# Kernel optimization log

Hardware: AMD Instinct MI355X
Metric: run time of the kernel (lower is better)

## Reference

```python
import jax, jax.numpy as jnp
import numpy as np

B, T, C, H = 2, 2048, 1024, 16
HD = C // H          # head dim = 64
HD2 = HD // 2        # rotary half = 32


def setup_inputs() -> dict:
    key = jax.random.key(0)
    k0, k1, k2 = jax.random.split(key, 3)
    x = jax.random.normal(k0, (B, T, C), jnp.float32)
    Wqkv = jax.random.normal(k1, (C, 3 * C), jnp.float32) * (1.0 / np.sqrt(C))
    bqkv = jnp.zeros((3 * C,), jnp.float32)
    Wproj = jax.random.normal(k2, (C, C), jnp.float32) * (1.0 / np.sqrt(C))
    bproj = jnp.zeros((C,), jnp.float32)
    # standard rotary frequencies: theta_i = 10000^{-2i/hd}
    inv_freq = 1.0 / (10000.0 ** (jnp.arange(0, HD, 2, dtype=jnp.float32) / HD))
    angles = jnp.arange(T, dtype=jnp.float32)[:, None] * inv_freq[None, :]  # (T, HD2)
    return {
        "x": x,
        "freqs_cos": jnp.cos(angles),
        "freqs_sin": jnp.sin(angles),
        "Wqkv": Wqkv,
        "bqkv": bqkv,
        "Wproj": Wproj,
        "bproj": bproj,
    }


def _rope(u, cos, sin):
    # u: (B, T, H, HD); half-split pairing: (u[i], u[i + HD/2]) form a complex pair
    u1, u2 = u[..., :HD2], u[..., HD2:]
    c = cos[None, :, None, :]  # (1, T, 1, HD2)
    s = sin[None, :, None, :]
    return jnp.concatenate([u1 * c - u2 * s, u1 * s + u2 * c], axis=-1)


def reference(x, freqs_cos, freqs_sin, Wqkv, bqkv, Wproj, bproj):
    Bc, Tc, Cc = x.shape
    qkv = x @ Wqkv + bqkv                      # (B, T, 3C)
    q, k, v = jnp.split(qkv, 3, axis=-1)
    q = q.reshape(Bc, Tc, H, HD)
    k = k.reshape(Bc, Tc, H, HD)
    v = v.reshape(Bc, Tc, H, HD)
    q = _rope(q, freqs_cos, freqs_sin)
    k = _rope(k, freqs_cos, freqs_sin)
    scale = 1.0 / np.sqrt(HD)
    scores = jnp.einsum("bthd,bshd->bhts", q, k) * scale  # (B, H, T, T)
    causal = jnp.tril(jnp.ones((Tc, Tc), dtype=bool))
    scores = jnp.where(causal[None, None], scores, jnp.finfo(scores.dtype).min)
    p = jax.nn.softmax(scores, axis=-1)
    y = jnp.einsum("bhts,bshd->bthd", p, v).reshape(Bc, Tc, Cc)
    return y @ Wproj + bproj
```

## Files before the change

kernel.cpp:

```cpp
#include <hip/hip_runtime.h>
#include <hip/hip_bf16.h>
#include <cstdint>
#include <cmath>

typedef __bf16 bf16_t;
typedef __attribute__((ext_vector_type(8))) __bf16 bf16x8;
typedef __attribute__((ext_vector_type(4))) float f32x4;

#define LOG2E 1.4426950408889634f

constexpr int B_ = 2, T_ = 2048, C_ = 1024, H_ = 16, HD_ = 64, HD2_ = 32;
constexpr int M_ = B_ * T_;

static __device__ __forceinline__ f32x4 mfma16(bf16x8 a, bf16x8 b, f32x4 c) {
    return __builtin_amdgcn_mfma_f32_16x16x32_bf16(a, b, c, 0, 0, 0);
}

#define GLL(gp, lp)                                                          \
    __builtin_amdgcn_global_load_lds(                                        \
        (const __attribute__((address_space(1))) void*)(gp),                 \
        (__attribute__((address_space(3))) void*)(lp), 16, 0, 0)

__global__ void cast_f32_to_bf16(const float* __restrict__ in, bf16_t* __restrict__ out, int n4) {
    int i = blockIdx.x * blockDim.x + threadIdx.x;
    if (i < n4) {
        float4 v = ((const float4*)in)[i];
        bf16_t o[4] = {(bf16_t)v.x, (bf16_t)v.y, (bf16_t)v.z, (bf16_t)v.w};
        *(uint64_t*)(out + (size_t)i * 4) = *(uint64_t*)o;
    }
}

__global__ void transpose_cast(const float* __restrict__ W, bf16_t* __restrict__ WT, int K, int N) {
    __shared__ float tile[32][33];
    int nb = blockIdx.x * 32, kb = blockIdx.y * 32;
    for (int i = threadIdx.y; i < 32; i += 8)
        tile[i][threadIdx.x] = W[(size_t)(kb + i) * N + nb + threadIdx.x];
    __syncthreads();
    for (int i = threadIdx.y; i < 32; i += 8)
        WT[(size_t)(nb + i) * K + kb + threadIdx.x] = (bf16_t)tile[threadIdx.x][i];
}

template <int MODE>
__global__ __launch_bounds__(256, 2) void gemm128(
    const bf16_t* __restrict__ A, const bf16_t* __restrict__ BT, const float* __restrict__ bias,
    int N, int K,
    bf16_t* __restrict__ Qb, bf16_t* __restrict__ Kb, bf16_t* __restrict__ VTb,
    const float* __restrict__ cosT, const float* __restrict__ sinT, float* __restrict__ out) {
    __shared__ alignas(16) bf16_t As[128 * 32];
    __shared__ alignas(16) bf16_t Bs[128 * 32];
    const int tid = threadIdx.x;
    const int w = tid >> 6, lane = tid & 63;
    const int quad = lane >> 4, r = lane & 15;
    const int wm = (w >> 1) * 64, wn = (w & 1) * 64;
    const int mb = blockIdx.y * 128, nb = blockIdx.x * 128;
    const int row_st = tid >> 2, seg = tid & 3;

    f32x4 acc[4][4] = {};

    const bf16_t* gA0 = A + (size_t)(mb + row_st) * K + seg * 8;
    const bf16_t* gA1 = A + (size_t)(mb + row_st + 64) * K + seg * 8;
    const bf16_t* gB0 = BT + (size_t)(nb + row_st) * K + seg * 8;
    const bf16_t* gB1 = BT + (size_t)(nb + row_st + 64) * K + seg * 8;

    for (int k0 = 0; k0 < K; k0 += 32) {
        __syncthreads();
        GLL(gA0 + k0, As + tid * 8);
        GLL(gA1 + k0, As + 2048 + tid * 8);
        GLL(gB0 + k0, Bs + tid * 8);
        GLL(gB1 + k0, Bs + 2048 + tid * 8);
        __syncthreads();
        bf16x8 af[4], bfr[4];
#pragma unroll
        for (int i = 0; i < 4; i++) af[i] = *(const bf16x8*)(As + (wm + i * 16 + r) * 32 + quad * 8);
#pragma unroll
        for (int j = 0; j < 4; j++) bfr[j] = *(const bf16x8*)(Bs + (wn + j * 16 + r) * 32 + quad * 8);
#pragma unroll
        for (int i = 0; i < 4; i++)
#pragma unroll
            for (int j = 0; j < 4; j++) acc[i][j] = mfma16(af[i], bfr[j], acc[i][j]);
    }

    if (MODE == 0) {
        const int col_base = nb + wn;
        const int region = col_base >> 10;
        const int h = (col_base & 1023) >> 6;
        const float qscale = 0.125f * LOG2E;
        if (region < 2) {
#pragma unroll
            for (int i = 0; i < 4; i++) {
#pragma unroll
                for (int g = 0; g < 4; g++) {
                    int m = mb + wm + i * 16 + quad * 4 + g;
                    int b = m >> 11, t = m & (T_ - 1);
                    bf16_t* dst = (region == 0 ? Qb : Kb) + ((size_t)((b * H_ + h) * T_ + t)) * 64;
                    int tw = t & 7;
#pragma unroll
                    for (int j = 0; j < 2; j++) {
                        int d = j * 16 + r;
                        float u1 = acc[i][j][g] + bias[col_base + d];
                        float u2 = acc[i][j + 2][g] + bias[col_base + d + 32];
                        float c = cosT[t * HD2_ + d], s = sinT[t * HD2_ + d];
                        float o1 = u1 * c - u2 * s;
                        float o2 = u1 * s + u2 * c;
                        if (region == 0) {
                            dst[d] = (bf16_t)(o1 * qscale);
                            dst[d + 32] = (bf16_t)(o2 * qscale);
                        } else {
                            dst[((((d >> 3) ^ tw)) << 3) | (d & 7)] = (bf16_t)o1;
                            dst[(((((d + 32) >> 3) ^ tw)) << 3) | (d & 7)] = (bf16_t)o2;
                        }
                    }
                }
            }
        } else {
#pragma unroll
            for (int i = 0; i < 4; i++) {
                int m0 = mb + wm + i * 16 + quad * 4;
                int b = m0 >> 11, t0 = m0 & (T_ - 1);
                bf16_t* base = VTb + (size_t)(b * H_ + h) * 64 * T_;
#pragma unroll
                for (int j = 0; j < 4; j++) {
                    int d = j * 16 + r;
                    float bb = bias[col_base + d];
                    bf16_t pk[4];
#pragma unroll
                    for (int g = 0; g < 4; g++) pk[g] = (bf16_t)(acc[i][j][g] + bb);
                    int c = (((t0 >> 3) & 7) ^ (d & 7));
                    int tsw = (t0 & ~63) | (c << 3) | (t0 & 7);
                    *(uint64_t*)(base + (size_t)d * T_ + tsw) = *(uint64_t*)pk;
                }
            }
        }
    } else {
#pragma unroll
        for (int i = 0; i < 4; i++)
#pragma unroll
            for (int g = 0; g < 4; g++) {
                int m = mb + wm + i * 16 + quad * 4 + g;
#pragma unroll
                for (int j = 0; j < 4; j++) {
                    int col = nb + wn + j * 16 + r;
                    out[(size_t)m * N + col] = acc[i][j][g] + bias[col];
                }
            }
    }
}

__global__ __launch_bounds__(256, 2) void attn64(
    const bf16_t* __restrict__ Qb, const bf16_t* __restrict__ Kb,
    const bf16_t* __restrict__ VTb, bf16_t* __restrict__ att) {
    __shared__ alignas(16) bf16_t Ks[2][64 * 64];
    __shared__ alignas(16) bf16_t Vs[2][64 * 64];
    __shared__ alignas(16) bf16_t Ps[4][1024];
    const int tid = threadIdx.x;
    const int w = tid >> 6, lane = tid & 63;
    const int quad = lane >> 4, r = lane & 15;
    const int pt = blockIdx.x;
    const int bh = blockIdx.y;
    const size_t kbase = (size_t)bh * T_ * 64;
    const size_t vbase = (size_t)bh * 64 * T_;
    bf16_t* Pw = &Ps[w][0];
    const int srow = tid >> 3, schunk = tid & 7;
    const int koff0 = ((quad ^ (r & 7)) * 8);
    const int koff1 = (((quad + 4) ^ (r & 7)) * 8);

    for (int half = 0; half < 2; half++) {
        const int qt = half ? (31 - pt) : pt;
        const int q0 = qt * 64;
        const int qrow = q0 + w * 16 + r;
        bf16x8 qf0 = *(const bf16x8*)(Qb + kbase + (size_t)qrow * 64 + quad * 8);
        bf16x8 qf1 = *(const bf16x8*)(Qb + kbase + (size_t)qrow * 64 + 32 + quad * 8);
        f32x4 oacc[4] = {};
        float mstate = -INFINITY, lstate = 0.f;
        const int n = qt + 1;

        __syncthreads();
        {
            const bf16_t* kg = Kb + kbase + (size_t)srow * 64 + schunk * 8;
            GLL(kg, &Ks[0][0] + tid * 8);
            GLL(kg + 32 * 64, &Ks[0][0] + 2048 + tid * 8);
            const bf16_t* vg = VTb + vbase + (size_t)srow * T_ + schunk * 8;
            GLL(vg, &Vs[0][0] + tid * 8);
            GLL(vg + (size_t)32 * T_, &Vs[0][0] + 2048 + tid * 8);
        }
        for (int jt = 0; jt < n; jt++) {
            const int cur = jt & 1;
            const int j0 = jt * 64;
            __syncthreads();
            if (jt + 1 < n) {
                const int j0n = j0 + 64;
                const bf16_t* kg = Kb + kbase + (size_t)(j0n + srow) * 64 + schunk * 8;
                GLL(kg, &Ks[cur ^ 1][0] + tid * 8);
                GLL(kg + 32 * 64, &Ks[cur ^ 1][0] + 2048 + tid * 8);
                const bf16_t* vg = VTb + vbase + (size_t)srow * T_ + j0n + schunk * 8;
                GLL(vg, &Vs[cur ^ 1][0] + tid * 8);
                GLL(vg + (size_t)32 * T_, &Vs[cur ^ 1][0] + 2048 + tid * 8);
            }
            f32x4 s[4];
#pragma unroll
            for (int m0 = 0; m0 < 4; m0++) {
                const bf16_t* kp = &Ks[cur][(m0 * 16 + r) * 64];
                bf16x8 kf0 = *(const bf16x8*)(kp + koff0);
                bf16x8 kf1 = *(const bf16x8*)(kp + koff1);
                f32x4 z = {0.f, 0.f, 0.f, 0.f};
                z = mfma16(kf0, qf0, z);
                z = mfma16(kf1, qf1, z);
                s[m0] = z;
            }
            if (jt == qt) {
#pragma unroll
                for (int m0 = 0; m0 < 4; m0++) {
                    int kvb = j0 + m0 * 16 + quad * 4;
#pragma unroll
                    for (int g = 0; g < 4; g++)
                        if (kvb + g > qrow) s[m0][g] = -INFINITY;
                }
            }
            float vm = -INFINITY;
#pragma unroll
            for (int m0 = 0; m0 < 4; m0++)
#pragma unroll
                for (int g = 0; g < 4; g++) vm = fmaxf(vm, s[m0][g]);
            vm = fmaxf(vm, __shfl_xor(vm, 16));
            vm = fmaxf(vm, __shfl_xor(vm, 32));
            float mnew = fmaxf(mstate, vm);
            float alpha = __builtin_amdgcn_exp2f(mstate - mnew);
            float rs = 0.f;
#pragma unroll
            for (int m0 = 0; m0 < 4; m0++)
#pragma unroll
                for (int g = 0; g < 4; g++) {
                    float p = __builtin_amdgcn_exp2f(s[m0][g] - mnew);
                    s[m0][g] = p;
                    rs += p;
                }
            rs += __shfl_xor(rs, 16);
            rs += __shfl_xor(rs, 32);
            lstate = lstate * alpha + rs;
            mstate = mnew;
#pragma unroll
            for (int d0 = 0; d0 < 4; d0++)
#pragma unroll
                for (int g = 0; g < 4; g++) oacc[d0][g] *= alpha;
#pragma unroll
            for (int m0 = 0; m0 < 4; m0++) {
                bf16_t hq[4];
#pragma unroll
                for (int g = 0; g < 4; g++) hq[g] = (bf16_t)s[m0][g];
                int elem = (m0 >> 1) * 512 + (((m0 & 1) * 2 + (quad >> 1)) * 16 + r) * 8 + (quad & 1) * 4;
                *(uint64_t*)(Pw + elem) = *(uint64_t*)hq;
            }
            __builtin_amdgcn_wave_barrier();
            bf16x8 pf0 = *(const bf16x8*)(Pw + lane * 8);
            bf16x8 pf1 = *(const bf16x8*)(Pw + 512 + lane * 8);
#pragma unroll
            for (int d0 = 0; d0 < 4; d0++) {
                const bf16_t* vp = &Vs[cur][(d0 * 16 + r) * 64];
                bf16x8 vf0 = *(const bf16x8*)(vp + koff0);
                bf16x8 vf1 = *(const bf16x8*)(vp + koff1);
                oacc[d0] = mfma16(vf0, pf0, oacc[d0]);
                oacc[d0] = mfma16(vf1, pf1, oacc[d0]);
            }
            __builtin_amdgcn_wave_barrier();
        }
        int b = bh >> 4, h = bh & 15;
        float inv = 1.f / lstate;
        bf16_t* dst = att + ((size_t)(b * T_ + qrow)) * 1024 + h * 64;
#pragma unroll
        for (int d0 = 0; d0 < 4; d0++) {
            bf16_t hh[4];
#pragma unroll
            for (int g = 0; g < 4; g++) hh[g] = (bf16_t)(oacc[d0][g] * inv);
            *(uint64_t*)(dst + d0 * 16 + quad * 4) = *(uint64_t*)hh;
        }
    }
}

extern "C" void kernel_launch(void* const* d_in, const int* in_sizes, int n_in,
                              void* d_out, int out_size, void* d_ws, size_t ws_size,
                              hipStream_t stream) {
    const float* x = (const float*)d_in[0];
    const float* fcos = (const float*)d_in[1];
    const float* fsin = (const float*)d_in[2];
    const float* Wqkv = (const float*)d_in[3];
    const float* bqkv = (const float*)d_in[4];
    const float* Wproj = (const float*)d_in[5];
    const float* bproj = (const float*)d_in[6];
    float* out = (float*)d_out;

    uint8_t* p = (uint8_t*)d_ws;
    size_t need = 0;
    auto take = [&](size_t bytes) {
        void* q = p;
        size_t pad = (bytes + 255) & ~(size_t)255;
        p += pad;
        need += pad;
        return q;
    };
    bf16_t* xb = (bf16_t*)take((size_t)M_ * C_ * 2);
    bf16_t* wqkvT = (bf16_t*)take((size_t)3 * C_ * C_ * 2);
    bf16_t* wprojT = (bf16_t*)take((size_t)C_ * C_ * 2);
    bf16_t* Qb = (bf16_t*)take((size_t)B_ * H_ * T_ * 64 * 2);
    bf16_t* Kb = (bf16_t*)take((size_t)B_ * H_ * T_ * 64 * 2);
    bf16_t* VTb = (bf16_t*)take((size_t)B_ * H_ * 64 * T_ * 2);
    bf16_t* attb = (bf16_t*)take((size_t)M_ * C_ * 2);
    if (ws_size < need) return;

    cast_f32_to_bf16<<<(M_ * C_ / 4 + 255) / 256, 256, 0, stream>>>(x, xb, M_ * C_ / 4);
    transpose_cast<<<dim3(3 * C_ / 32, C_ / 32), dim3(32, 8), 0, stream>>>(Wqkv, wqkvT, C_, 3 * C_);
    transpose_cast<<<dim3(C_ / 32, C_ / 32), dim3(32, 8), 0, stream>>>(Wproj, wprojT, C_, C_);

    gemm128<0><<<dim3(3 * C_ / 128, M_ / 128), 256, 0, stream>>>(
        xb, wqkvT, bqkv, 3 * C_, C_, Qb, Kb, VTb, fcos, fsin, nullptr);

    attn64<<<dim3(16, B_ * H_), 256, 0, stream>>>(Qb, Kb, VTb, attb);

    gemm128<1><<<dim3(C_ / 128, M_ / 128), 256, 0, stream>>>(
        attb, wprojT, bproj, C_, C_, nullptr, nullptr, nullptr, nullptr, nullptr, out);
}
```

Before: 204.7 us.

## Process paired query tiles together in attention and merge prep kernels

The attention kernel now handles its two causal-balanced query tiles (pt and 31-pt) in one shared pass over K/V tiles. Each staged K/V tile is reused for both query tiles, so the shorter tile's K/V loads and barriers are no longer repeated. The grid is flattened and remapped so that the heads sharing an XCD index are grouped, which is meant to improve L2 locality. The three preprocessing kernels (x cast and two weight transposes) are merged into one launch. In exchange, each thread holds more live registers for two sets of accumulators, and the P scratch buffer in LDS doubles.

```diff
diff --git a/kernel.cpp b/kernel.cpp
--- a/kernel.cpp
+++ b/kernel.cpp
@@ -21,23 +21,36 @@
         (const __attribute__((address_space(1))) void*)(gp),                 \
         (__attribute__((address_space(3))) void*)(lp), 16, 0, 0)
 
-__global__ void cast_f32_to_bf16(const float* __restrict__ in, bf16_t* __restrict__ out, int n4) {
-    int i = blockIdx.x * blockDim.x + threadIdx.x;
-    if (i < n4) {
-        float4 v = ((const float4*)in)[i];
+__global__ void prep(const float* __restrict__ x, bf16_t* __restrict__ xb,
+                     const float* __restrict__ Wqkv, bf16_t* __restrict__ wqkvT,
+                     const float* __restrict__ Wproj, bf16_t* __restrict__ wprojT) {
+    __shared__ float tile[32][33];
+    const int bid = blockIdx.x, tid = threadIdx.x;
+    if (bid < 4096) {
+        int i = bid * 256 + tid;
+        float4 v = ((const float4*)x)[i];
         bf16_t o[4] = {(bf16_t)v.x, (bf16_t)v.y, (bf16_t)v.z, (bf16_t)v.w};
-        *(uint64_t*)(out + (size_t)i * 4) = *(uint64_t*)o;
-    }
-}
-
-__global__ void transpose_cast(const float* __restrict__ W, bf16_t* __restrict__ WT, int K, int N) {
-    __shared__ float tile[32][33];
-    int nb = blockIdx.x * 32, kb = blockIdx.y * 32;
-    for (int i = threadIdx.y; i < 32; i += 8)
-        tile[i][threadIdx.x] = W[(size_t)(kb + i) * N + nb + threadIdx.x];
+        *(uint64_t*)(xb + (size_t)i * 4) = *(uint64_t*)o;
+        return;
+    }
+    const float* W;
+    bf16_t* WT;
+    int K, N, nb, kb;
+    if (bid < 4096 + 3072) {
+        int t = bid - 4096;
+        W = Wqkv; WT = wqkvT; K = C_; N = 3 * C_;
+        nb = (t % 96) * 32; kb = (t / 96) * 32;
+    } else {
+        int t = bid - 7168;
+        W = Wproj; WT = wprojT; K = C_; N = C_;
+        nb = (t & 31) * 32; kb = (t >> 5) * 32;
+    }
+    int tx = tid & 31, ty = tid >> 5;
+    for (int i = ty; i < 32; i += 8)
+        tile[i][tx] = W[(size_t)(kb + i) * N + nb + tx];
     __syncthreads();
-    for (int i = threadIdx.y; i < 32; i += 8)
-        WT[(size_t)(nb + i) * K + kb + threadIdx.x] = (bf16_t)tile[threadIdx.x][i];
+    for (int i = ty; i < 32; i += 8)
+        WT[(size_t)(nb + i) * K + kb + tx] = (bf16_t)tile[tx][i];
 }
 
 template <int MODE>
@@ -151,126 +164,186 @@
     const bf16_t* __restrict__ VTb, bf16_t* __restrict__ att) {
     __shared__ alignas(16) bf16_t Ks[2][64 * 64];
     __shared__ alignas(16) bf16_t Vs[2][64 * 64];
-    __shared__ alignas(16) bf16_t Ps[4][1024];
+    __shared__ alignas(16) bf16_t Ps[4][2048];
     const int tid = threadIdx.x;
     const int w = tid >> 6, lane = tid & 63;
     const int quad = lane >> 4, r = lane & 15;
-    const int pt = blockIdx.x;
-    const int bh = blockIdx.y;
+    const int idx = blockIdx.x;
+    const int xcd = idx & 7, jj = idx >> 3;
+    const int bh = (jj >> 4) * 8 + xcd;
+    const int pt = jj & 15;
+    const int qtA = pt, qtB = 31 - pt;
     const size_t kbase = (size_t)bh * T_ * 64;
     const size_t vbase = (size_t)bh * 64 * T_;
-    bf16_t* Pw = &Ps[w][0];
+    bf16_t* PwB = &Ps[w][0];
+    bf16_t* PwA = &Ps[w][1024];
     const int srow = tid >> 3, schunk = tid & 7;
     const int koff0 = ((quad ^ (r & 7)) * 8);
     const int koff1 = (((quad + 4) ^ (r & 7)) * 8);
 
-    for (int half = 0; half < 2; half++) {
-        const int qt = half ? (31 - pt) : pt;
-        const int q0 = qt * 64;
-        const int qrow = q0 + w * 16 + r;
-        bf16x8 qf0 = *(const bf16x8*)(Qb + kbase + (size_t)qrow * 64 + quad * 8);
-        bf16x8 qf1 = *(const bf16x8*)(Qb + kbase + (size_t)qrow * 64 + 32 + quad * 8);
-        f32x4 oacc[4] = {};
-        float mstate = -INFINITY, lstate = 0.f;
-        const int n = qt + 1;
-
+    const int qrowA = qtA * 64 + w * 16 + r;
+    const int qrowB = qtB * 64 + w * 16 + r;
+    bf16x8 qfA0 = *(const bf16x8*)(Qb + kbase + (size_t)qrowA * 64 + quad * 8);
+    bf16x8 qfA1 = *(const bf16x8*)(Qb + kbase + (size_t)qrowA * 64 + 32 + quad * 8);
+    bf16x8 qfB0 = *(const bf16x8*)(Qb + kbase + (size_t)qrowB * 64 + quad * 8);
+    bf16x8 qfB1 = *(const bf16x8*)(Qb + kbase + (size_t)qrowB * 64 + 32 + quad * 8);
+
+    f32x4 oaccA[4] = {}, oaccB[4] = {};
+    float mA = -INFINITY, lA = 0.f, mB = -INFINITY, lB = 0.f;
+
+    auto stageKV = [&](int jt, int buf) {
+        const bf16_t* kg = Kb + kbase + (size_t)(jt * 64 + srow) * 64 + schunk * 8;
+        GLL(kg, &Ks[buf][0] + tid * 8);
+        GLL(kg + 32 * 64, &Ks[buf][0] + 2048 + tid * 8);
+        const bf16_t* vg = VTb + vbase + (size_t)srow * T_ + jt * 64 + schunk * 8;
+        GLL(vg, &Vs[buf][0] + tid * 8);
+        GLL(vg + (size_t)32 * T_, &Vs[buf][0] + 2048 + tid * 8);
+    };
+    auto softmax = [&](f32x4* s, float& m, float& l, f32x4* oacc) {
+        float vm = -INFINITY;
+#pragma unroll
+        for (int m0 = 0; m0 < 4; m0++)
+#pragma unroll
+            for (int g = 0; g < 4; g++) vm = fmaxf(vm, s[m0][g]);
+        vm = fmaxf(vm, __shfl_xor(vm, 16));
+        vm = fmaxf(vm, __shfl_xor(vm, 32));
+        float mnew = fmaxf(m, vm);
+        float alpha = __builtin_amdgcn_exp2f(m - mnew);
+        float rs = 0.f;
+#pragma unroll
+        for (int m0 = 0; m0 < 4; m0++)
+#pragma unroll
+            for (int g = 0; g < 4; g++) {
+                float pp = __builtin_amdgcn_exp2f(s[m0][g] - mnew);
+                s[m0][g] = pp;
+                rs += pp;
+            }
+        rs += __shfl_xor(rs, 16);
+        rs += __shfl_xor(rs, 32);
+        l = l * alpha + rs;
+        m = mnew;
+#pragma unroll
+        for (int d0 = 0; d0 < 4; d0++)
+#pragma unroll
+            for (int g = 0; g < 4; g++) oacc[d0][g] *= alpha;
+    };
+    auto packP = [&](f32x4* s, bf16_t* Pw) {
+#pragma unroll
+        for (int m0 = 0; m0 < 4; m0++) {
+            bf16_t hq[4];
+#pragma unroll
+            for (int g = 0; g < 4; g++) hq[g] = (bf16_t)s[m0][g];
+            int elem = (m0 >> 1) * 512 + (((m0 & 1) * 2 + (quad >> 1)) * 16 + r) * 8 + (quad & 1) * 4;
+            *(uint64_t*)(Pw + elem) = *(uint64_t*)hq;
+        }
+    };
+
+    stageKV(0, 0);
+    for (int jt = 0; jt <= qtB; jt++) {
+        const int cur = jt & 1;
+        const int j0 = jt * 64;
         __syncthreads();
-        {
-            const bf16_t* kg = Kb + kbase + (size_t)srow * 64 + schunk * 8;
-            GLL(kg, &Ks[0][0] + tid * 8);
-            GLL(kg + 32 * 64, &Ks[0][0] + 2048 + tid * 8);
-            const bf16_t* vg = VTb + vbase + (size_t)srow * T_ + schunk * 8;
-            GLL(vg, &Vs[0][0] + tid * 8);
-            GLL(vg + (size_t)32 * T_, &Vs[0][0] + 2048 + tid * 8);
-        }
-        for (int jt = 0; jt < n; jt++) {
-            const int cur = jt & 1;
-            const int j0 = jt * 64;
-            __syncthreads();
-            if (jt + 1 < n) {
-                const int j0n = j0 + 64;
-                const bf16_t* kg = Kb + kbase + (size_t)(j0n + srow) * 64 + schunk * 8;
-                GLL(kg, &Ks[cur ^ 1][0] + tid * 8);
-                GLL(kg + 32 * 64, &Ks[cur ^ 1][0] + 2048 + tid * 8);
-                const bf16_t* vg = VTb + vbase + (size_t)srow * T_ + j0n + schunk * 8;
-                GLL(vg, &Vs[cur ^ 1][0] + tid * 8);
-                GLL(vg + (size_t)32 * T_, &Vs[cur ^ 1][0] + 2048 + tid * 8);
-            }
-            f32x4 s[4];
+        if (jt < qtB) stageKV(jt + 1, cur ^ 1);
+        const bool doA = (jt <= qtA);
+
+        f32x4 sA[4], sB[4];
+        if (doA) {
 #pragma unroll
             for (int m0 = 0; m0 < 4; m0++) {
                 const bf16_t* kp = &Ks[cur][(m0 * 16 + r) * 64];
                 bf16x8 kf0 = *(const bf16x8*)(kp + koff0);
                 bf16x8 kf1 = *(const bf16x8*)(kp + koff1);
-                f32x4 z = {0.f, 0.f, 0.f, 0.f};
-                z = mfma16(kf0, qf0, z);
-                z = mfma16(kf1, qf1, z);
-                s[m0] = z;
-            }
-            if (jt == qt) {
-#pragma unroll
-                for (int m0 = 0; m0 < 4; m0++) {
-                    int kvb = j0 + m0 * 16 + quad * 4;
-#pragma unroll
-                    for (int g = 0; g < 4; g++)
-                        if (kvb + g > qrow) s[m0][g] = -INFINITY;
-                }
-            }
-            float vm = -INFINITY;
-#pragma unroll
-            for (int m0 = 0; m0 < 4; m0++)
-#pragma unroll
-                for (int g = 0; g < 4; g++) vm = fmaxf(vm, s[m0][g]);
-            vm = fmaxf(vm, __shfl_xor(vm, 16));
-            vm = fmaxf(vm, __shfl_xor(vm, 32));
-            float mnew = fmaxf(mstate, vm);
-            float alpha = __builtin_amdgcn_exp2f(mstate - mnew);
-            float rs = 0.f;
-#pragma unroll
-            for (int m0 = 0; m0 < 4; m0++)
-#pragma unroll
-                for (int g = 0; g < 4; g++) {
-                    float p = __builtin_amdgcn_exp2f(s[m0][g] - mnew);
-                    s[m0][g] = p;
-                    rs += p;
-                }
-            rs += __shfl_xor(rs, 16);
-            rs += __shfl_xor(rs, 32);
-            lstate = lstate * alpha + rs;
-            mstate = mnew;
-#pragma unroll
-            for (int d0 = 0; d0 < 4; d0++)
-#pragma unroll
-                for (int g = 0; g < 4; g++) oacc[d0][g] *= alpha;
+                f32x4 zB = {0.f, 0.f, 0.f, 0.f};
+                zB = mfma16(kf0, qfB0, zB);
+                zB = mfma16(kf1, qfB1, zB);
+                sB[m0] = zB;
+                f32x4 zA = {0.f, 0.f, 0.f, 0.f};
+                zA = mfma16(kf0, qfA0, zA);
+                zA = mfma16(kf1, qfA1, zA);
+                sA[m0] = zA;
+            }
+        } else {
 #pragma unroll
             for (int m0 = 0; m0 < 4; m0++) {
-                bf16_t hq[4];
-#pragma unroll
-                for (int g = 0; g < 4; g++) hq[g] = (bf16_t)s[m0][g];
-                int elem = (m0 >> 1) * 512 + (((m0 & 1) * 2 + (quad >> 1)) * 16 + r) * 8 + (quad & 1) * 4;
-                *(uint64_t*)(Pw + elem) = *(uint64_t*)hq;
-            }
-            __builtin_amdgcn_wave_barrier();
-            bf16x8 pf0 = *(const bf16x8*)(Pw + lane * 8);
-            bf16x8 pf1 = *(const bf16x8*)(Pw + 512 + lane * 8);
+                const bf16_t* kp = &Ks[cur][(m0 * 16 + r) * 64];
+                bf16x8 kf0 = *(const bf16x8*)(kp + koff0);
+                bf16x8 kf1 = *(const bf16x8*)(kp + koff1);
+                f32x4 zB = {0.f, 0.f, 0.f, 0.f};
+                zB = mfma16(kf0, qfB0, zB);
+                zB = mfma16(kf1, qfB1, zB);
+                sB[m0] = zB;
+            }
+        }
+        if (jt == qtB) {
+#pragma unroll
+            for (int m0 = 0; m0 < 4; m0++) {
+                int kvb = j0 + m0 * 16 + quad * 4;
+#pragma unroll
+                for (int g = 0; g < 4; g++)
+                    if (kvb + g > qrowB) sB[m0][g] = -INFINITY;
+            }
+        }
+        if (jt == qtA) {
+#pragma unroll
+            for (int m0 = 0; m0 < 4; m0++) {
+                int kvb = j0 + m0 * 16 + quad * 4;
+#pragma unroll
+                for (int g = 0; g < 4; g++)
+                    if (kvb + g > qrowA) sA[m0][g] = -INFINITY;
+            }
+        }
+        softmax(sB, mB, lB, oaccB);
+        if (doA) softmax(sA, mA, lA, oaccA);
+        packP(sB, PwB);
+        if (doA) packP(sA, PwA);
+        __builtin_amdgcn_wave_barrier();
+        bf16x8 pfB0 = *(const bf16x8*)(PwB + lane * 8);
+        bf16x8 pfB1 = *(const bf16x8*)(PwB + 512 + lane * 8);
+        if (doA) {
+            bf16x8 pfA0 = *(const bf16x8*)(PwA + lane * 8);
+            bf16x8 pfA1 = *(const bf16x8*)(PwA + 512 + lane * 8);
 #pragma unroll
             for (int d0 = 0; d0 < 4; d0++) {
                 const bf16_t* vp = &Vs[cur][(d0 * 16 + r) * 64];
                 bf16x8 vf0 = *(const bf16x8*)(vp + koff0);
                 bf16x8 vf1 = *(const bf16x8*)(vp + koff1);
-                oacc[d0] = mfma16(vf0, pf0, oacc[d0]);
-                oacc[d0] = mfma16(vf1, pf1, oacc[d0]);
-            }
-            __builtin_amdgcn_wave_barrier();
-        }
-        int b = bh >> 4, h = bh & 15;
-        float inv = 1.f / lstate;
-        bf16_t* dst = att + ((size_t)(b * T_ + qrow)) * 1024 + h * 64;
+                oaccB[d0] = mfma16(vf0, pfB0, oaccB[d0]);
+                oaccB[d0] = mfma16(vf1, pfB1, oaccB[d0]);
+                oaccA[d0] = mfma16(vf0, pfA0, oaccA[d0]);
+                oaccA[d0] = mfma16(vf1, pfA1, oaccA[d0]);
+            }
+        } else {
+#pragma unroll
+            for (int d0 = 0; d0 < 4; d0++) {
+                const bf16_t* vp = &Vs[cur][(d0 * 16 + r) * 64];
+                bf16x8 vf0 = *(const bf16x8*)(vp + koff0);
+                bf16x8 vf1 = *(const bf16x8*)(vp + koff1);
+                oaccB[d0] = mfma16(vf0, pfB0, oaccB[d0]);
+                oaccB[d0] = mfma16(vf1, pfB1, oaccB[d0]);
+            }
+        }
+        __builtin_amdgcn_wave_barrier();
+    }
+    const int b = bh >> 4, h = bh & 15;
+    {
+        float inv = 1.f / lB;
+        bf16_t* dst = att + ((size_t)(b * T_ + qrowB)) * 1024 + h * 64;
 #pragma unroll
         for (int d0 = 0; d0 < 4; d0++) {
             bf16_t hh[4];
 #pragma unroll
-            for (int g = 0; g < 4; g++) hh[g] = (bf16_t)(oacc[d0][g] * inv);
+            for (int g = 0; g < 4; g++) hh[g] = (bf16_t)(oaccB[d0][g] * inv);
+            *(uint64_t*)(dst + d0 * 16 + quad * 4) = *(uint64_t*)hh;
+        }
+    }
+    {
+        float inv = 1.f / lA;
+        bf16_t* dst = att + ((size_t)(b * T_ + qrowA)) * 1024 + h * 64;
+#pragma unroll
+        for (int d0 = 0; d0 < 4; d0++) {
+            bf16_t hh[4];
+#pragma unroll
+            for (int g = 0; g < 4; g++) hh[g] = (bf16_t)(oaccA[d0][g] * inv);
             *(uint64_t*)(dst + d0 * 16 + quad * 4) = *(uint64_t*)hh;
         }
     }
@@ -306,14 +379,12 @@
     bf16_t* attb = (bf16_t*)take((size_t)M_ * C_ * 2);
     if (ws_size < need) return;
 
-    cast_f32_to_bf16<<<(M_ * C_ / 4 + 255) / 256, 256, 0, stream>>>(x, xb, M_ * C_ / 4);
-    transpose_cast<<<dim3(3 * C_ / 32, C_ / 32), dim3(32, 8), 0, stream>>>(Wqkv, wqkvT, C_, 3 * C_);
-    transpose_cast<<<dim3(C_ / 32, C_ / 32), dim3(32, 8), 0, stream>>>(Wproj, wprojT, C_, C_);
+    prep<<<8192, 256, 0, stream>>>(x, xb, Wqkv, wqkvT, Wproj, wprojT);
 
     gemm128<0><<<dim3(3 * C_ / 128, M_ / 128), 256, 0, stream>>>(
         xb, wqkvT, bqkv, 3 * C_, C_, Qb, Kb, VTb, fcos, fsin, nullptr);
 
-    attn64<<<dim3(16, B_ * H_), 256, 0, stream>>>(Qb, Kb, VTb, attb);
+    attn64<<<dim3(512), 256, 0, stream>>>(Qb, Kb, VTb, attb);
 
     gemm128<1><<<dim3(C_ / 128, M_ / 128), 256, 0, stream>>>(
         attb, wprojT, bproj, C_, C_, nullptr, nullptr, nullptr, nullptr, nullptr, out);
```

After: 200.3 us. 1.02x faster.
